# Kernel tuning notes

Hardware: AMD Instinct MI355X
Metric: run time of the kernel (lower is better)

The kernel has to match this reference:

```python
import jax, jax.numpy as jnp
import numpy as np

C = 512
HSIZE = C // 4
D, H, W = 18, 24, 24
N = D * H * W


def setup_inputs() -> dict:
    key = jax.random.key(0)
    ks = jax.random.split(key, 6)
    features = jax.random.normal(ks[0], (1, C, D, H, W), dtype=jnp.float32)
    Wi = jax.random.normal(ks[1], (HSIZE, C), dtype=jnp.float32) * 0.02
    bi = jax.random.normal(ks[2], (HSIZE,), dtype=jnp.float32) * 0.02
    Wj = jax.random.normal(ks[3], (HSIZE, C), dtype=jnp.float32) * 0.02
    bj = jax.random.normal(ks[4], (HSIZE,), dtype=jnp.float32) * 0.02
    # attention_agregate: shape (head=1, 1), xavier-uniform in the original
    agg = jax.random.uniform(ks[5], (1, 1), dtype=jnp.float32, minval=-1.0, maxval=1.0)
    return {"features": features, "Wi": Wi, "bi": bi, "Wj": Wj, "bj": bj, "agg": agg}


def reference(features, Wi, bi, Wj, bj, agg):
    # features: [1, C, D, H, W]; 1x1x1 convs == channel-wise matmuls
    x = features.reshape(C, N)                      # [C, N]
    fi = (Wi @ x + bi[:, None]).T                   # [N, hsize]  (conv_i output, permuted)
    fj = Wj @ x + bj[:, None]                       # [hsize, N]  (conv_j output)
    fk = x.T                                        # [N, C]      (raw features, NOT conv_k)
    # original: attn = (fi @ fj) * agg / N ; out = attn @ fk
    # linear chain reassociated: fi @ (fj @ fk) * agg / N  (same math, no NxN intermediate)
    scale = agg[0, 0] / jnp.float32(N)
    out_flat = (fi @ (fj @ fk)) * scale             # [N, C]
    return features + out_flat.T.reshape(1, C, D, H, W)
```

## Files before the change

kernel.cpp:

```cpp
#include <hip/hip_runtime.h>
#include <hip/hip_bf16.h>

#define C_   512
#define HS   128
#define NN   10368

typedef __bf16 bf16x8 __attribute__((ext_vector_type(8)));
typedef __bf16 bf16x4 __attribute__((ext_vector_type(4)));
typedef __bf16 bf16x2 __attribute__((ext_vector_type(2)));
typedef float  f32x4  __attribute__((ext_vector_type(4)));

__device__ __forceinline__ bf16x8 load_f32x8_as_bf16(const float* __restrict__ p) {
    float4 v0 = *(const float4*)p;
    float4 v1 = *(const float4*)(p + 4);
    bf16x8 o;
    o[0] = (__bf16)v0.x; o[1] = (__bf16)v0.y; o[2] = (__bf16)v0.z; o[3] = (__bf16)v0.w;
    o[4] = (__bf16)v1.x; o[5] = (__bf16)v1.y; o[6] = (__bf16)v1.z; o[7] = (__bf16)v1.w;
    return o;
}

__global__ __launch_bounds__(256, 2)
void k_prep(const float* __restrict__ Wi, const float* __restrict__ Wj,
            __bf16* __restrict__ Wib, __bf16* __restrict__ Wjb,
            float* __restrict__ Mtf) {
    const int b = blockIdx.x;
    const int t = threadIdx.x;
    if (b < 4) {
        const float* src = (b < 2) ? Wj : Wi;
        __bf16* dst = (b < 2) ? Wjb : Wib;
        const int off = (b & 1) * 32768;
        #pragma unroll 4
        for (int u = 0; u < 32; u++) {
            const int idx = off + u * 1024 + t * 4;
            float4 v = *(const float4*)(src + idx);
            bf16x4 o;
            o[0] = (__bf16)v.x; o[1] = (__bf16)v.y;
            o[2] = (__bf16)v.z; o[3] = (__bf16)v.w;
            *(bf16x4*)(dst + idx) = o;
        }
    } else {
        const int z = b - 4;
        f32x4 zv = {0.f, 0.f, 0.f, 0.f};
        float* p = Mtf + z * 4096 + t * 16;
        *(f32x4*)(p) = zv; *(f32x4*)(p + 4) = zv;
        *(f32x4*)(p + 8) = zv; *(f32x4*)(p + 12) = zv;
    }
}

__global__ __launch_bounds__(256, 2)
void k_fused12(const float* __restrict__ feat,
               const __bf16* __restrict__ Wib, const __bf16* __restrict__ Wjb,
               const float* __restrict__ bi, const float* __restrict__ bj,
               __bf16* __restrict__ xb, __bf16* __restrict__ fj,
               __bf16* __restrict__ finm) {
    const int b = blockIdx.x;
    const int t = threadIdx.x;
    __shared__ __bf16 xt[16][520];
    const int n0 = b * 16;
    {
        const int g  = t & 3;
        const int c8 = t >> 2;
        const int nq = 4 * g;
        #pragma unroll
        for (int p = 0; p < 8; p++) {
            const int c = c8 + 64 * p;
            float4 v = *(const float4*)(feat + (size_t)c * NN + n0 + nq);
            bf16x4 o;
            o[0] = (__bf16)v.x; o[1] = (__bf16)v.y;
            o[2] = (__bf16)v.z; o[3] = (__bf16)v.w;
            *(bf16x4*)(xb + (size_t)c * NN + n0 + nq) = o;
            xt[nq + 0][c] = o[0];
            xt[nq + 1][c] = o[1];
            xt[nq + 2][c] = o[2];
            xt[nq + 3][c] = o[3];
        }
    }
    __syncthreads();
    const int w    = t >> 6;
    const int lane = t & 63;
    const int l16  = lane & 15;
    const int q    = lane >> 4;
    const int h0   = w * 32;
    f32x4 afj[2] = {};
    f32x4 afi[2] = {};
    #pragma unroll 4
    for (int k = 0; k < 512; k += 32) {
        bf16x8 ln, wj[2], wi[2];
        ln = *(const bf16x8*)&xt[l16][k + q * 8];
        #pragma unroll
        for (int i = 0; i < 2; i++)
            wj[i] = *(const bf16x8*)&Wjb[(size_t)(h0 + 16 * i + l16) * C_ + k + q * 8];
        #pragma unroll
        for (int i = 0; i < 2; i++)
            wi[i] = *(const bf16x8*)&Wib[(size_t)(h0 + 16 * i + l16) * C_ + k + q * 8];
        #pragma unroll
        for (int i = 0; i < 2; i++) {
            afj[i] = __builtin_amdgcn_mfma_f32_16x16x32_bf16(wj[i], ln, afj[i], 0, 0, 0);
            afi[i] = __builtin_amdgcn_mfma_f32_16x16x32_bf16(ln, wi[i], afi[i], 0, 0, 0);
        }
    }
    float4 bjv[2];
    bjv[0] = *(const float4*)(bj + h0 + q * 4);
    bjv[1] = *(const float4*)(bj + h0 + 16 + q * 4);
    float biv[2];
    biv[0] = bi[h0 + l16];
    biv[1] = bi[h0 + 16 + l16];
    #pragma unroll
    for (int i = 0; i < 2; i++)
        #pragma unroll
        for (int r = 0; r < 4; r++) {
            {
                int h = h0 + 16 * i + q * 4 + r;
                int n = n0 + l16;
                fj[(size_t)h * NN + n] = (__bf16)(afj[i][r] + (&bjv[i].x)[r]);
            }
            {
                int n = n0 + q * 4 + r;
                int h = h0 + 16 * i + l16;
                finm[(size_t)n * HS + h] = (__bf16)(afi[i][r] + biv[i]);
            }
        }
}

__global__ __launch_bounds__(256, 2)
void k_gemm3(const __bf16* __restrict__ xb, const __bf16* __restrict__ fj,
             float* __restrict__ Mtf) {
    __shared__ float red[4][64][17];
    const int b    = blockIdx.x;
    const int t    = threadIdx.x;
    const int v    = t >> 6;
    const int lane = t & 63;
    const int l16  = lane & 15;
    const int q    = lane >> 4;
    const int tile = b & 63, g = b >> 6;
    const int c0 = (tile >> 2) * 32, h0 = (tile & 3) * 32;
    const int chunk = g * 4 + v;
    const int s0 = (chunk * 324) >> 5;
    const int s1 = ((chunk + 1) * 324) >> 5;
    f32x4 acc[2][2] = {};
    bf16x8 a[2], bb[2];
    {
        const int k = s0 * 32;
        a[0]  = *(const bf16x8*)(xb + (size_t)(c0 + l16) * NN + k + q * 8);
        a[1]  = *(const bf16x8*)(xb + (size_t)(c0 + 16 + l16) * NN + k + q * 8);
        bb[0] = *(const bf16x8*)(fj + (size_t)(h0 + l16) * NN + k + q * 8);
        bb[1] = *(const bf16x8*)(fj + (size_t)(h0 + 16 + l16) * NN + k + q * 8);
    }
    for (int s = s0; s < s1 - 1; s++) {
        const int kn = (s + 1) * 32;
        bf16x8 a2[2], b2[2];
        a2[0] = *(const bf16x8*)(xb + (size_t)(c0 + l16) * NN + kn + q * 8);
        a2[1] = *(const bf16x8*)(xb + (size_t)(c0 + 16 + l16) * NN + kn + q * 8);
        b2[0] = *(const bf16x8*)(fj + (size_t)(h0 + l16) * NN + kn + q * 8);
        b2[1] = *(const bf16x8*)(fj + (size_t)(h0 + 16 + l16) * NN + kn + q * 8);
        #pragma unroll
        for (int i = 0; i < 2; i++)
            #pragma unroll
            for (int tt = 0; tt < 2; tt++)
                acc[i][tt] = __builtin_amdgcn_mfma_f32_16x16x32_bf16(a[i], bb[tt], acc[i][tt], 0, 0, 0);
        a[0] = a2[0]; a[1] = a2[1]; bb[0] = b2[0]; bb[1] = b2[1];
    }
    #pragma unroll
    for (int i = 0; i < 2; i++)
        #pragma unroll
        for (int tt = 0; tt < 2; tt++)
            acc[i][tt] = __builtin_amdgcn_mfma_f32_16x16x32_bf16(a[i], bb[tt], acc[i][tt], 0, 0, 0);
    #pragma unroll
    for (int i = 0; i < 2; i++)
        #pragma unroll
        for (int tt = 0; tt < 2; tt++)
            #pragma unroll
            for (int r = 0; r < 4; r++)
                red[v][lane][i * 8 + tt * 4 + r] = acc[i][tt][r];
    __syncthreads();
    #pragma unroll
    for (int u = 0; u < 4; u++) {
        const int idx = t * 4 + u;
        const int lane_e = idx >> 4, j = idx & 15;
        float s = red[0][lane_e][j] + red[1][lane_e][j]
                + red[2][lane_e][j] + red[3][lane_e][j];
        const int i = j >> 3, tt = (j >> 2) & 1, r = j & 3;
        const int qe = lane_e >> 4, le = lane_e & 15;
        const int c = c0 + 16 * i + qe * 4 + r;
        const int h = h0 + 16 * tt + le;
        atomicAdd(&Mtf[c * HS + h], s);
    }
}

__global__ __launch_bounds__(256, 2)
void k_gemm4(const float* __restrict__ Mtf, const __bf16* __restrict__ finm,
             const float* __restrict__ feat, const float* __restrict__ agg,
             float* __restrict__ out) {
    __shared__ float lds_out[128][64];
    const int t    = threadIdx.x;
    const int wv   = t >> 6;
    const int w    = blockIdx.x * 4 + wv;
    const int lane = t & 63;
    const int l16  = lane & 15;
    const int q    = lane >> 4;
    const int c0 = (w & 15) * 32, n0 = (w >> 4) * 64;
    const float scale = agg[0] * (1.0f / (float)NN);
    f32x4 acc[2][4] = {};
    #pragma unroll
    for (int k = 0; k < 128; k += 32) {
        bf16x8 a[2], bfr[4];
        #pragma unroll
        for (int i = 0; i < 2; i++)
            a[i] = load_f32x8_as_bf16(Mtf + (c0 + 16 * i + l16) * HS + k + q * 8);
        #pragma unroll
        for (int tt = 0; tt < 4; tt++)
            bfr[tt] = *(const bf16x8*)(finm + (size_t)(n0 + 16 * tt + l16) * HS + k + q * 8);
        #pragma unroll
        for (int i = 0; i < 2; i++)
            #pragma unroll
            for (int tt = 0; tt < 4; tt++)
                acc[i][tt] = __builtin_amdgcn_mfma_f32_16x16x32_bf16(a[i], bfr[tt], acc[i][tt], 0, 0, 0);
    }
    #pragma unroll
    for (int i = 0; i < 2; i++)
        #pragma unroll
        for (int tt = 0; tt < 4; tt++)
            #pragma unroll
            for (int r = 0; r < 4; r++)
                lds_out[wv * 32 + 16 * i + q * 4 + r][16 * tt + l16] = scale * acc[i][tt][r];
    __syncthreads();
    const int c0b = ((blockIdx.x * 4) & 15) * 32;
    const int n0b = ((blockIdx.x * 4) >> 4) * 64;
    #pragma unroll
    for (int rr = 0; rr < 2; rr++) {
        const int row = (t >> 2) + 64 * rr;
        const size_t gbase = (size_t)(c0b + row) * NN + n0b;
        float4 fv[4];
        #pragma unroll
        for (int j4 = 0; j4 < 4; j4++) {
            const int col = (t & 3) * 4 + j4 * 16;
            fv[j4] = *(const float4*)(feat + gbase + col);
        }
        #pragma unroll
        for (int j4 = 0; j4 < 4; j4++) {
            const int col = (t & 3) * 4 + j4 * 16;
            f32x4 v = *(const f32x4*)&lds_out[row][col];
            float4 o;
            o.x = fv[j4].x + v[0]; o.y = fv[j4].y + v[1];
            o.z = fv[j4].z + v[2]; o.w = fv[j4].w + v[3];
            *(float4*)(out + gbase + col) = o;
        }
    }
}

extern "C" void kernel_launch(void* const* d_in, const int* in_sizes, int n_in,
                              void* d_out, int out_size, void* d_ws, size_t ws_size,
                              hipStream_t stream) {
    const float* feat = (const float*)d_in[0];
    const float* Wi   = (const float*)d_in[1];
    const float* bi   = (const float*)d_in[2];
    const float* Wj   = (const float*)d_in[3];
    const float* bj   = (const float*)d_in[4];
    const float* agg  = (const float*)d_in[5];
    float* out = (float*)d_out;

    char* ws = (char*)d_ws;
    __bf16* xb   = (__bf16*)(ws);
    __bf16* fj   = (__bf16*)(ws + 10616832);
    __bf16* finm = (__bf16*)(ws + 13271040);
    float*  Mtf  = (float*) (ws + 15925248);
    __bf16* Wjb  = (__bf16*)(ws + 16187392);
    __bf16* Wib  = (__bf16*)(ws + 16318464);

    k_prep   <<<20,  256, 0, stream>>>(Wi, Wj, Wib, Wjb, Mtf);
    k_fused12<<<648, 256, 0, stream>>>(feat, Wib, Wjb, bi, bj, xb, fj, finm);
    k_gemm3  <<<512, 256, 0, stream>>>(xb, fj, Mtf);
    k_gemm4  <<<648, 256, 0, stream>>>(Mtf, finm, feat, agg, out);
}
```

Baseline: 138.4 us.

## Retile fused projection kernel to 32 positions per block with 8 waves

The fused conv_i/conv_j projection kernel now handles 32 spatial positions per block with 512 threads (8 waves) instead of 16 positions with 4 waves. Each wave covers 16 output channels over two 16-position tiles, so every weight fragment loaded from global memory feeds two MFMAs. This halves the per-position weight traffic and the block count. In exchange the block is larger with more shared memory, and fewer blocks may reduce occupancy and load balance across CUs.

```diff
diff --git a/kernel.cpp b/kernel.cpp
--- a/kernel.cpp
+++ b/kernel.cpp
@@ -47,7 +47,7 @@
     }
 }
 
-__global__ __launch_bounds__(256, 2)
+__global__ __launch_bounds__(512, 2)
 void k_fused12(const float* __restrict__ feat,
                const __bf16* __restrict__ Wib, const __bf16* __restrict__ Wjb,
                const float* __restrict__ bi, const float* __restrict__ bj,
@@ -55,11 +55,11 @@
                __bf16* __restrict__ finm) {
     const int b = blockIdx.x;
     const int t = threadIdx.x;
-    __shared__ __bf16 xt[16][520];
-    const int n0 = b * 16;
+    __shared__ __bf16 xt[32][520];
+    const int n0 = b * 32;
     {
-        const int g  = t & 3;
-        const int c8 = t >> 2;
+        const int g  = t & 7;
+        const int c8 = t >> 3;
         const int nq = 4 * g;
         #pragma unroll
         for (int p = 0; p < 8; p++) {
@@ -80,45 +80,37 @@
     const int lane = t & 63;
     const int l16  = lane & 15;
     const int q    = lane >> 4;
-    const int h0   = w * 32;
+    const int h0   = w * 16;
     f32x4 afj[2] = {};
     f32x4 afi[2] = {};
     #pragma unroll 4
     for (int k = 0; k < 512; k += 32) {
-        bf16x8 ln, wj[2], wi[2];
-        ln = *(const bf16x8*)&xt[l16][k + q * 8];
-        #pragma unroll
-        for (int i = 0; i < 2; i++)
-            wj[i] = *(const bf16x8*)&Wjb[(size_t)(h0 + 16 * i + l16) * C_ + k + q * 8];
-        #pragma unroll
-        for (int i = 0; i < 2; i++)
-            wi[i] = *(const bf16x8*)&Wib[(size_t)(h0 + 16 * i + l16) * C_ + k + q * 8];
-        #pragma unroll
-        for (int i = 0; i < 2; i++) {
-            afj[i] = __builtin_amdgcn_mfma_f32_16x16x32_bf16(wj[i], ln, afj[i], 0, 0, 0);
-            afi[i] = __builtin_amdgcn_mfma_f32_16x16x32_bf16(ln, wi[i], afi[i], 0, 0, 0);
-        }
-    }
-    float4 bjv[2];
-    bjv[0] = *(const float4*)(bj + h0 + q * 4);
-    bjv[1] = *(const float4*)(bj + h0 + 16 + q * 4);
-    float biv[2];
-    biv[0] = bi[h0 + l16];
-    biv[1] = bi[h0 + 16 + l16];
-    #pragma unroll
-    for (int i = 0; i < 2; i++)
+        bf16x8 ln0 = *(const bf16x8*)&xt[l16][k + q * 8];
+        bf16x8 ln1 = *(const bf16x8*)&xt[16 + l16][k + q * 8];
+        bf16x8 wjf = *(const bf16x8*)&Wjb[(size_t)(h0 + l16) * C_ + k + q * 8];
+        bf16x8 wif = *(const bf16x8*)&Wib[(size_t)(h0 + l16) * C_ + k + q * 8];
+        afj[0] = __builtin_amdgcn_mfma_f32_16x16x32_bf16(wjf, ln0, afj[0], 0, 0, 0);
+        afj[1] = __builtin_amdgcn_mfma_f32_16x16x32_bf16(wjf, ln1, afj[1], 0, 0, 0);
+        afi[0] = __builtin_amdgcn_mfma_f32_16x16x32_bf16(ln0, wif, afi[0], 0, 0, 0);
+        afi[1] = __builtin_amdgcn_mfma_f32_16x16x32_bf16(ln1, wif, afi[1], 0, 0, 0);
+    }
+    const float4 bjv = *(const float4*)(bj + h0 + q * 4);
+    const float  biv = bi[h0 + l16];
+    #pragma unroll
+    for (int tt = 0; tt < 2; tt++)
         #pragma unroll
         for (int r = 0; r < 4; r++) {
-            {
-                int h = h0 + 16 * i + q * 4 + r;
-                int n = n0 + l16;
-                fj[(size_t)h * NN + n] = (__bf16)(afj[i][r] + (&bjv[i].x)[r]);
-            }
-            {
-                int n = n0 + q * 4 + r;
-                int h = h0 + 16 * i + l16;
-                finm[(size_t)n * HS + h] = (__bf16)(afi[i][r] + biv[i]);
-            }
+            const int h = h0 + q * 4 + r;
+            const int n = n0 + 16 * tt + l16;
+            fj[(size_t)h * NN + n] = (__bf16)(afj[tt][r] + (&bjv.x)[r]);
+        }
+    #pragma unroll
+    for (int i2 = 0; i2 < 2; i2++)
+        #pragma unroll
+        for (int r = 0; r < 4; r++) {
+            const int n = n0 + 16 * i2 + q * 4 + r;
+            const int h = h0 + l16;
+            finm[(size_t)n * HS + h] = (__bf16)(afi[i2][r] + biv);
         }
 }
 
@@ -268,7 +260,7 @@
     __bf16* Wib  = (__bf16*)(ws + 16318464);
 
     k_prep   <<<20,  256, 0, stream>>>(Wi, Wj, Wib, Wjb, Mtf);
-    k_fused12<<<648, 256, 0, stream>>>(feat, Wib, Wjb, bi, bj, xb, fj, finm);
+    k_fused12<<<324, 512, 0, stream>>>(feat, Wib, Wjb, bi, bj, xb, fj, finm);
     k_gemm3  <<<512, 256, 0, stream>>>(xb, fj, Mtf);
     k_gemm4  <<<648, 256, 0, stream>>>(Mtf, finm, feat, agg, out);
 }
```

New measurement: 129.6 us. 6.3% less time.
